# Kernel optimization log

Hardware: AMD Instinct MI355X
Metric: run time of the kernel (lower is better)

Reference implementation:

```python
import jax, jax.numpy as jnp
import numpy as np
from jax import lax

B_, L, D, EXPAND, N, R, K = 2, 1024, 1024, 2, 16, 64, 4
ED = EXPAND * D


def setup_inputs() -> dict:
    key = jax.random.key(0)
    ks = jax.random.split(key, 8)
    x = jax.random.normal(ks[0], (B_, L, D), dtype=jnp.float32)
    in_proj_w = jax.random.normal(ks[1], (2 * ED, D), dtype=jnp.float32) * (D ** -0.5)
    in_proj_b = jnp.zeros((2 * ED,), jnp.float32)
    conv_w = jax.random.normal(ks[2], (ED, 1, K), dtype=jnp.float32) * (K ** -0.5)
    conv_b = jnp.zeros((ED,), jnp.float32)
    x_proj_w = jax.random.normal(ks[3], (R + 2 * N, ED), dtype=jnp.float32) * (ED ** -0.5)
    dt_proj_w = jax.random.uniform(ks[4], (ED, R), jnp.float32, -(R ** -0.5), R ** -0.5)
    # inverse-softplus of dt ~ U[log(dt_min), log(dt_max)] (matches torch init)
    dt = jnp.exp(jax.random.uniform(ks[5], (ED,), jnp.float32) * (np.log(0.1) - np.log(0.001)) + np.log(0.001))
    dt_proj_b = dt + jnp.log(-jnp.expm1(-dt))  # softplus^{-1}(dt)
    A_log = jnp.log(jnp.broadcast_to(jnp.arange(1, N + 1, dtype=jnp.float32), (ED, N)))
    D_param = jnp.ones((ED,), jnp.float32)
    out_proj_w = jax.random.normal(ks[6], (D, ED), dtype=jnp.float32) * (ED ** -0.5)
    return {"x": x, "in_proj_w": in_proj_w, "in_proj_b": in_proj_b, "conv_w": conv_w,
            "conv_b": conv_b, "x_proj_w": x_proj_w, "dt_proj_w": dt_proj_w,
            "dt_proj_b": dt_proj_b, "A_log": A_log, "D_param": D_param,
            "out_proj_w": out_proj_w}


def _mamba_fwd(x, in_proj_w, in_proj_b, conv_w, conv_b, x_proj_w, dt_proj_w,
               dt_proj_b, A_log, D_param, out_proj_w):
    xz = x @ in_proj_w.T + in_proj_b                       # (B, L, 2*ED)
    xc, z = jnp.split(xz, 2, axis=-1)                      # (B, L, ED) each
    # causal depthwise conv over time (pad left K-1, valid)
    xc = xc.transpose(0, 2, 1)                             # (B, ED, L)
    xc = lax.conv_general_dilated(xc, conv_w, window_strides=(1,),
                                  padding=[(K - 1, 0)], feature_group_count=ED)
    xc = xc + conv_b[None, :, None]
    xc = jax.nn.silu(xc.transpose(0, 2, 1))                # (B, L, ED)
    # SSM params
    A = -jnp.exp(A_log)                                    # (ED, N)
    dbc = xc @ x_proj_w.T                                  # (B, L, R+2N)
    dt, Bmat, Cmat = jnp.split(dbc, [R, R + N], axis=-1)
    dt = jax.nn.softplus(dt @ dt_proj_w.T + dt_proj_b)     # (B, L, ED)
    dA = jnp.exp(dt[..., None] * A)                        # (B, L, ED, N)
    dBx = (dt * xc)[..., None] * Bmat[:, :, None, :]       # (B, L, ED, N)
    # parallel scan: h_t = dA_t * h_{t-1} + dBx_t
    def combine(e1, e2):
        a1, b1 = e1
        a2, b2 = e2
        return a1 * a2, a2 * b1 + b2
    _, hs = lax.associative_scan(combine, (dA, dBx), axis=1)  # (B, L, ED, N)
    y = jnp.einsum('bln,blen->ble', Cmat, hs) + D_param * xc  # (B, L, ED)
    out = (y * jax.nn.silu(z)) @ out_proj_w.T                 # (B, L, D)
    return out


def reference(x, in_proj_w, in_proj_b, conv_w, conv_b, x_proj_w, dt_proj_w,
              dt_proj_b, A_log, D_param, out_proj_w):
    return _mamba_fwd(x, in_proj_w, in_proj_b, conv_w, conv_b, x_proj_w,
                      dt_proj_w, dt_proj_b, A_log, D_param, out_proj_w)
```

## Files before the change

kernel.cpp:

```cpp
#include <hip/hip_runtime.h>
#include <cstddef>


#define BL   2048
#define DIM  1024
#define ED   2048
#define NST  16
#define RLOW 64
#define CH   64
#define LC   16
#define SK   16
#define DBCN 196608

typedef __attribute__((ext_vector_type(4))) float   f32x4;
typedef __attribute__((ext_vector_type(8))) __bf16  bf16x8;
typedef __attribute__((ext_vector_type(8))) unsigned short us8;

__device__ __forceinline__ float silu_(float x) {
  return x / (1.f + __expf(-x));
}

__device__ __forceinline__ unsigned short f2b(float x) {
  union { float f; unsigned int u; } v; v.f = x;
  unsigned int r = v.u + 0x7FFFu + ((v.u >> 16) & 1u);
  return (unsigned short)(r >> 16);
}

__device__ __forceinline__ float b2f(unsigned short u) {
  union { unsigned int i; float f; } v; v.i = (unsigned int)u << 16; return v.f;
}

__device__ __forceinline__ f32x4 mfma_bf16(us8 a, us8 b, f32x4 c) {
  return __builtin_amdgcn_mfma_f32_16x16x32_bf16(
      __builtin_bit_cast(bf16x8, a), __builtin_bit_cast(bf16x8, b), c, 0, 0, 0);
}

#define GLOAD_LDS16(gaddr, laddr)                                              \
  __builtin_amdgcn_global_load_lds(                                            \
      (const __attribute__((address_space(1))) unsigned int*)(gaddr),          \
      (__attribute__((address_space(3))) unsigned int*)(laddr), 16, 0, 0)

template <int BM, int BN, bool OBF>
__global__ __launch_bounds__(256) void gemm_bf16(
    const unsigned short* __restrict__ A,
    const unsigned short* __restrict__ W,
    const float* __restrict__ bias,
    void* __restrict__ Cp, int ldc, int Nout, int Kloop, int lda, int sstride)
{
  constexpr int BK  = 32;
  constexpr int FM  = BM / 32;
  constexpr int FN  = BN / 32;
  constexpr int NLA = BM / 64;
  constexpr int NLW = BN / 64;
  __shared__ unsigned short Alds[BM][BK];
  __shared__ unsigned short Wlds[BN][BK];

  const int tid  = threadIdx.x;
  const int w    = tid >> 6;
  const int lane = tid & 63;
  const int wr   = w >> 1, wc = w & 1;
  const int bm   = blockIdx.x * BM;
  const int bn   = blockIdx.y * BN;
  const int kb   = blockIdx.z * Kloop;

  f32x4 acc[FM][FN];
#pragma unroll
  for (int m = 0; m < FM; ++m)
#pragma unroll
    for (int n = 0; n < FN; ++n) acc[m][n] = (f32x4){0.f, 0.f, 0.f, 0.f};

  const int srow = w * 16 + (lane & 15);
  const int kq   = (lane >> 4) * 8;

  for (int k0 = 0; k0 < Kloop; k0 += BK) {
    __syncthreads();
#pragma unroll
    for (int j = 0; j < NLA; ++j)
      GLOAD_LDS16(A + (size_t)(bm + j * 64 + srow) * lda + kb + k0 + kq,
                  &Alds[j * 64 + w * 16][0]);
#pragma unroll
    for (int j = 0; j < NLW; ++j)
      GLOAD_LDS16(W + (size_t)(bn + j * 64 + srow) * lda + kb + k0 + kq,
                  &Wlds[j * 64 + w * 16][0]);
    __syncthreads();
    us8 af[FM], wf[FN];
#pragma unroll
    for (int m = 0; m < FM; ++m)
      af[m] = *(const us8*)(&Alds[0][0] + (wr * (BM / 2) + m * 16) * BK + lane * 8);
#pragma unroll
    for (int n = 0; n < FN; ++n)
      wf[n] = *(const us8*)(&Wlds[0][0] + (wc * (BN / 2) + n * 16) * BK + lane * 8);
#pragma unroll
    for (int m = 0; m < FM; ++m)
#pragma unroll
      for (int n = 0; n < FN; ++n)
        acc[m][n] = mfma_bf16(af[m], wf[n], acc[m][n]);
  }

  const int rbase = (lane >> 4) * 4;
  float* Cf = (float*)Cp + (size_t)blockIdx.z * sstride;
#pragma unroll
  for (int m = 0; m < FM; ++m) {
#pragma unroll
    for (int n = 0; n < FN; ++n) {
      const int col = bn + wc * (BN / 2) + n * 16 + (lane & 15);
      if (col < Nout) {
        const float bv = bias ? bias[col] : 0.f;
#pragma unroll
        for (int r = 0; r < 4; ++r) {
          const int row = bm + wr * (BM / 2) + m * 16 + rbase + r;
          const float v = acc[m][n][r] + bv;
          if (OBF) ((unsigned short*)Cp)[(size_t)row * ldc + col] = f2b(v);
          else     Cf[(size_t)row * ldc + col] = v;
        }
      }
    }
  }
}

__global__ __launch_bounds__(256) void reduce_dbc_k(
    const float* __restrict__ par, float* __restrict__ dbc)
{
  const int i = blockIdx.x * 256 + threadIdx.x;
  float4 s = ((const float4*)par)[i];
#pragma unroll
  for (int sk = 1; sk < SK; ++sk) {
    float4 v = ((const float4*)(par + (size_t)sk * DBCN))[i];
    s.x += v.x; s.y += v.y; s.z += v.z; s.w += v.w;
  }
  ((float4*)dbc)[i] = s;
}

template <int ACT>
__global__ __launch_bounds__(256) void gemm_nt(
    const float* __restrict__ A, int lda,
    const float* __restrict__ W, int ldw,
    const float* __restrict__ bias,
    float* __restrict__ C, int ldc,
    int N, int K)
{
  __shared__ float As[16][64];
  __shared__ float Ws[16][64];
  const int tid = threadIdx.x;
  const int bm = blockIdx.x * 64;
  const int bn = blockIdx.y * 64;
  const int tx = tid & 15;
  const int ty = tid >> 4;
  const int srow = tid >> 2;
  const int scg  = (tid & 3) * 4;

  float acc[4][4] = {};
  const float* Aptr = A + (size_t)(bm + srow) * lda + scg;
  const bool   wok  = (bn + srow) < N;
  const float* Wptr = W + (size_t)(bn + srow) * ldw + scg;

  for (int k0 = 0; k0 < K; k0 += 16) {
    float4 av = *(const float4*)(Aptr + k0);
    float4 wv = make_float4(0.f, 0.f, 0.f, 0.f);
    if (wok) wv = *(const float4*)(Wptr + k0);
    __syncthreads();
    As[scg + 0][srow] = av.x; As[scg + 1][srow] = av.y;
    As[scg + 2][srow] = av.z; As[scg + 3][srow] = av.w;
    Ws[scg + 0][srow] = wv.x; Ws[scg + 1][srow] = wv.y;
    Ws[scg + 2][srow] = wv.z; Ws[scg + 3][srow] = wv.w;
    __syncthreads();
#pragma unroll
    for (int k = 0; k < 16; ++k) {
      float4 a4 = *(const float4*)&As[k][ty * 4];
      float4 w4 = *(const float4*)&Ws[k][tx * 4];
      float a_[4] = {a4.x, a4.y, a4.z, a4.w};
      float w_[4] = {w4.x, w4.y, w4.z, w4.w};
#pragma unroll
      for (int i = 0; i < 4; ++i)
#pragma unroll
        for (int j = 0; j < 4; ++j)
          acc[i][j] += a_[i] * w_[j];
    }
  }

#pragma unroll
  for (int i = 0; i < 4; ++i) {
    const int row = bm + ty * 4 + i;
#pragma unroll
    for (int j = 0; j < 4; ++j) {
      const int col = bn + tx * 4 + j;
      if (col < N) {
        float v = acc[i][j];
        if (bias) v += bias[col];
        if (ACT == 1) v = (v > 20.f) ? v : log1pf(__expf(v));
        C[(size_t)row * ldc + col] = v;
      }
    }
  }
}

__global__ __launch_bounds__(256) void cvt_bf16_k(
    const float* __restrict__ in, unsigned short* __restrict__ out, int n4)
{
  const int i = blockIdx.x * 256 + threadIdx.x;
  if (i >= n4) return;
  float4 v = ((const float4*)in)[i];
  ushort4 o;
  o.x = f2b(v.x); o.y = f2b(v.y); o.z = f2b(v.z); o.w = f2b(v.w);
  ((ushort4*)out)[i] = o;
}

__global__ __launch_bounds__(256) void cvt_pad_xpw_k(
    const float* __restrict__ in, unsigned short* __restrict__ out)
{
  const int i = blockIdx.x * 256 + threadIdx.x;
  const int idx = i * 4;
  const int row = idx >> 11;
  ushort4 o = {0, 0, 0, 0};
  if (row < 96) {
    float4 v = *(const float4*)(in + idx);
    o.x = f2b(v.x); o.y = f2b(v.y); o.z = f2b(v.z); o.w = f2b(v.w);
  }
  *(ushort4*)(out + idx) = o;
}

__global__ __launch_bounds__(256) void conv_silu_k(
    const unsigned short* __restrict__ xzb, const float* __restrict__ cw,
    const float* __restrict__ cb, unsigned short* __restrict__ xcb)
{
  const int idx = blockIdx.x * 256 + threadIdx.x;
  const int row = idx >> 9;
  const int e   = (idx & 511) * 4;
  const int l   = row & 1023;
  const unsigned short* base = xzb + (size_t)(row - l) * (2 * ED) + e;

  float4 cbv = *(const float4*)(cb + e);
  float a0 = cbv.x, a1 = cbv.y, a2 = cbv.z, a3 = cbv.w;
#pragma unroll
  for (int k = 0; k < 4; ++k) {
    const int ls = l - 3 + k;
    if (ls >= 0) {
      ushort4 u = *(const ushort4*)(base + (size_t)ls * (2 * ED));
      a0 += cw[(size_t)(e + 0) * 4 + k] * b2f(u.x);
      a1 += cw[(size_t)(e + 1) * 4 + k] * b2f(u.y);
      a2 += cw[(size_t)(e + 2) * 4 + k] * b2f(u.z);
      a3 += cw[(size_t)(e + 3) * 4 + k] * b2f(u.w);
    }
  }
  ushort4 o;
  o.x = f2b(silu_(a0)); o.y = f2b(silu_(a1));
  o.z = f2b(silu_(a2)); o.w = f2b(silu_(a3));
  *(ushort4*)(xcb + (size_t)row * ED + e) = o;
}

__global__ __launch_bounds__(256, 4) void scan_phase1(
    const float* __restrict__ dt, const unsigned short* __restrict__ xcb,
    const float* __restrict__ dbc, const float* __restrict__ A_log,
    float* __restrict__ aprod_o, float* __restrict__ bfin_o)
{
  const int g  = blockIdx.x * 256 + threadIdx.x;
  const int e  = g & (ED - 1);
  const int bc = g >> 11;
  const int b  = bc >> 6;
  const int c  = bc & (CH - 1);
  const size_t rowbase = (size_t)b * 1024 + (size_t)c * LC;

  __shared__ float4 sB[LC][4];
  if (threadIdx.x < LC * 4) {
    const int row = threadIdx.x >> 2, q = threadIdx.x & 3;
    sB[row][q] = ((const float4*)(dbc + (rowbase + row) * 96 + RLOW))[q];
  }
  __syncthreads();

  float Aen[NST];
  {
    const float4* Ap = (const float4*)(A_log + (size_t)e * NST);
#pragma unroll
    for (int q = 0; q < 4; ++q) {
      float4 v = Ap[q];
      Aen[q*4+0] = -__expf(v.x); Aen[q*4+1] = -__expf(v.y);
      Aen[q*4+2] = -__expf(v.z); Aen[q*4+3] = -__expf(v.w);
    }
  }

  float dtv[LC], dxv[LC];
#pragma unroll
  for (int i = 0; i < LC; ++i) dtv[i] = dt[(rowbase + i) * ED + e];
#pragma unroll
  for (int i = 0; i < LC; ++i)
    dxv[i] = dtv[i] * b2f(xcb[(rowbase + i) * ED + e]);

  float h[NST], ap[NST];
#pragma unroll
  for (int n = 0; n < NST; ++n) { h[n] = 0.f; ap[n] = 1.f; }

  for (int i = 0; i < LC; ++i) {
    float Bv[NST];
#pragma unroll
    for (int q = 0; q < 4; ++q) {
      float4 v = sB[i][q];
      Bv[q*4+0]=v.x; Bv[q*4+1]=v.y; Bv[q*4+2]=v.z; Bv[q*4+3]=v.w;
    }
#pragma unroll
    for (int n = 0; n < NST; ++n) {
      const float dA = __expf(dtv[i] * Aen[n]);
      ap[n] *= dA;
      h[n] = fmaf(dA, h[n], dxv[i] * Bv[n]);
    }
  }

  const size_t obase = ((size_t)(b * ED + e) * CH + c) * NST;
  float4* ao = (float4*)(aprod_o + obase);
  float4* bo = (float4*)(bfin_o + obase);
#pragma unroll
  for (int q = 0; q < 4; ++q) {
    ao[q] = make_float4(ap[q*4+0], ap[q*4+1], ap[q*4+2], ap[q*4+3]);
    bo[q] = make_float4(h[q*4+0],  h[q*4+1],  h[q*4+2],  h[q*4+3]);
  }
}

__global__ __launch_bounds__(256) void scan_phase2(
    const float* __restrict__ aprod, float* __restrict__ bfin)
{
  const int be   = blockIdx.x * 4 + (threadIdx.x >> 6);
  const int lane = threadIdx.x & 63;
  const size_t base = (size_t)be * CH * NST;

  float Aa[NST], Bb[NST];
  {
    const float4* ap4 = (const float4*)(aprod + base);
    const float4* bp4 = (const float4*)(bfin + base);
#pragma unroll
    for (int q = 0; q < 4; ++q) {
      float4 v = ap4[lane * 4 + q];
      Aa[q*4+0]=v.x; Aa[q*4+1]=v.y; Aa[q*4+2]=v.z; Aa[q*4+3]=v.w;
      float4 w = bp4[lane * 4 + q];
      Bb[q*4+0]=w.x; Bb[q*4+1]=w.y; Bb[q*4+2]=w.z; Bb[q*4+3]=w.w;
    }
  }

#pragma unroll
  for (int d = 1; d < 64; d <<= 1) {
#pragma unroll
    for (int r = 0; r < NST; ++r) {
      const float aP = __shfl_up(Aa[r], d);
      const float bP = __shfl_up(Bb[r], d);
      if (lane >= d) {
        Bb[r] = fmaf(Aa[r], bP, Bb[r]);
        Aa[r] *= aP;
      }
    }
  }

#pragma unroll
  for (int r = 0; r < NST; ++r) {
    const float hs = __shfl_up(Bb[r], 1);
    Bb[r] = (lane == 0) ? 0.f : hs;
  }

  float4* ob4 = (float4*)(bfin + base);
#pragma unroll
  for (int q = 0; q < 4; ++q)
    ob4[lane * 4 + q] = make_float4(Bb[q*4+0], Bb[q*4+1], Bb[q*4+2], Bb[q*4+3]);
}

__global__ __launch_bounds__(256, 4) void scan_phase3(
    const float* __restrict__ dt, const unsigned short* __restrict__ xcb,
    const float* __restrict__ dbc, const float* __restrict__ A_log,
    const float* __restrict__ Dp, const unsigned short* __restrict__ xzb,
    const float* __restrict__ hst, unsigned short* __restrict__ ygb)
{
  const int g  = blockIdx.x * 256 + threadIdx.x;
  const int e  = g & (ED - 1);
  const int bc = g >> 11;
  const int b  = bc >> 6;
  const int c  = bc & (CH - 1);
  const size_t rowbase = (size_t)b * 1024 + (size_t)c * LC;

  __shared__ float4 sBC[LC][8];
  if (threadIdx.x < LC * 8) {
    const int row = threadIdx.x >> 3, q = threadIdx.x & 7;
    sBC[row][q] = ((const float4*)(dbc + (rowbase + row) * 96 + RLOW))[q];
  }
  __syncthreads();

  float Aen[NST];
  {
    const float4* Ap = (const float4*)(A_log + (size_t)e * NST);
#pragma unroll
    for (int q = 0; q < 4; ++q) {
      float4 v = Ap[q];
      Aen[q*4+0] = -__expf(v.x); Aen[q*4+1] = -__expf(v.y);
      Aen[q*4+2] = -__expf(v.z); Aen[q*4+3] = -__expf(v.w);
    }
  }

  float dtv[LC], xcv[LC];
#pragma unroll
  for (int i = 0; i < LC; ++i) dtv[i] = dt[(rowbase + i) * ED + e];
#pragma unroll
  for (int i = 0; i < LC; ++i) xcv[i] = b2f(xcb[(rowbase + i) * ED + e]);

  float h[NST];
  {
    const float4* Hp = (const float4*)(hst + ((size_t)(b * ED + e) * CH + c) * NST);
#pragma unroll
    for (int q = 0; q < 4; ++q) {
      float4 v = Hp[q];
      h[q*4+0]=v.x; h[q*4+1]=v.y; h[q*4+2]=v.z; h[q*4+3]=v.w;
    }
  }

  const float De = Dp[e];
  for (int i = 0; i < LC; ++i) {
    const size_t rr = rowbase + i;
    float Bv[NST], Cv[NST];
#pragma unroll
    for (int q = 0; q < 4; ++q) {
      float4 v = sBC[i][q];
      Bv[q*4+0]=v.x; Bv[q*4+1]=v.y; Bv[q*4+2]=v.z; Bv[q*4+3]=v.w;
      float4 w = sBC[i][q + 4];
      Cv[q*4+0]=w.x; Cv[q*4+1]=w.y; Cv[q*4+2]=w.z; Cv[q*4+3]=w.w;
    }
    const float dx = dtv[i] * xcv[i];
    float y = 0.f;
#pragma unroll
    for (int n = 0; n < NST; ++n) {
      const float dA = __expf(dtv[i] * Aen[n]);
      h[n] = fmaf(dA, h[n], dx * Bv[n]);
      y = fmaf(Cv[n], h[n], y);
    }
    y = fmaf(De, xcv[i], y);
    const float zf = b2f(xzb[rr * (2 * ED) + ED + e]);
    ygb[rr * ED + e] = f2b(y * silu_(zf));
  }
}

extern "C" void kernel_launch(void* const* d_in, const int* in_sizes, int n_in,
                              void* d_out, int out_size, void* d_ws, size_t ws_size,
                              hipStream_t stream) {
  const float* x         = (const float*)d_in[0];
  const float* in_w      = (const float*)d_in[1];
  const float* in_b      = (const float*)d_in[2];
  const float* conv_w    = (const float*)d_in[3];
  const float* conv_b    = (const float*)d_in[4];
  const float* xproj_w   = (const float*)d_in[5];
  const float* dtproj_w  = (const float*)d_in[6];
  const float* dtproj_b  = (const float*)d_in[7];
  const float* A_log     = (const float*)d_in[8];
  const float* D_param   = (const float*)d_in[9];
  const float* outproj_w = (const float*)d_in[10];
  float* out = (float*)d_out;

  float* ws    = (float*)d_ws;
  float* dbc   = ws;
  float* dtb   = dbc   + 196608;
  float* aprod = dtb   + 4194304;
  float* bfin  = aprod + 4194304;
  float* par   = bfin  + 4194304;
  unsigned short* xzb  = (unsigned short*)(par + 3145728);
  unsigned short* xb   = xzb  + 8388608;
  unsigned short* iwb  = xb   + 2097152;
  unsigned short* owb  = iwb  + 4194304;
  unsigned short* xpwb = owb  + 2097152;
  unsigned short* xcb  = xpwb + 262144;
  unsigned short* ygb  = xcb  + 4194304;

  const dim3 blk(256);

  cvt_bf16_k<<<dim3(2097152 / 4 / 256), blk, 0, stream>>>(x, xb, 2097152 / 4);
  cvt_bf16_k<<<dim3(4194304 / 4 / 256), blk, 0, stream>>>(in_w, iwb, 4194304 / 4);
  cvt_bf16_k<<<dim3(2097152 / 4 / 256), blk, 0, stream>>>(outproj_w, owb, 2097152 / 4);
  cvt_pad_xpw_k<<<dim3(262144 / 4 / 256), blk, 0, stream>>>(xproj_w, xpwb);

  gemm_bf16<128, 128, true><<<dim3(BL / 128, 4096 / 128), blk, 0, stream>>>(
      xb, iwb, in_b, xzb, 2 * ED, 2 * ED, DIM, DIM, 0);

  conv_silu_k<<<dim3((BL * (ED / 4)) / 256), blk, 0, stream>>>(
      xzb, conv_w, conv_b, xcb);

  gemm_bf16<128, 128, false><<<dim3(BL / 128, 1, SK), blk, 0, stream>>>(
      xcb, xpwb, nullptr, par, 96, 96, ED / SK, ED, DBCN);
  reduce_dbc_k<<<dim3(DBCN / 4 / 256), blk, 0, stream>>>(par, dbc);

  gemm_nt<1><<<dim3(BL / 64, ED / 64), blk, 0, stream>>>(
      dbc, 96, dtproj_w, RLOW, dtproj_b, dtb, ED, ED, RLOW);

  scan_phase1<<<dim3((2 * CH * ED) / 256), blk, 0, stream>>>(
      dtb, xcb, dbc, A_log, aprod, bfin);
  scan_phase2<<<dim3((2 * ED) / 4), blk, 0, stream>>>(aprod, bfin);
  scan_phase3<<<dim3((2 * CH * ED) / 256), blk, 0, stream>>>(
      dtb, xcb, dbc, A_log, D_param, xzb, bfin, ygb);

  gemm_bf16<64, 64, false><<<dim3(BL / 64, 1024 / 64), blk, 0, stream>>>(
      ygb, owb, nullptr, out, DIM, DIM, ED, ED, 0);
}
```

Measured before the change: 232.4 us.

## Double-buffer bf16 GEMM with BK=64, fuse conversions, split-K out_proj

The bf16 MFMA GEMM now uses BK=64 with double-buffered LDS, so the global-to-LDS load of the next tile is issued before the MFMAs on the current tile, and each iteration needs one barrier instead of two. The four fp32-to-bf16 conversion kernels are merged into one launch. The out_proj GEMM uses 64x128 tiles with a 2-way split-K into scratch (reusing the aprod buffer), followed by a small reduction kernel. This adds LDS use per block, which may lower occupancy, and adds an extra partial-sum write and reduction pass for the output.

```diff
diff --git a/kernel.cpp b/kernel.cpp
--- a/kernel.cpp
+++ b/kernel.cpp
@@ -47,13 +47,14 @@
     const float* __restrict__ bias,
     void* __restrict__ Cp, int ldc, int Nout, int Kloop, int lda, int sstride)
 {
-  constexpr int BK  = 32;
-  constexpr int FM  = BM / 32;
-  constexpr int FN  = BN / 32;
-  constexpr int NLA = BM / 64;
-  constexpr int NLW = BN / 64;
-  __shared__ unsigned short Alds[BM][BK];
-  __shared__ unsigned short Wlds[BN][BK];
+  constexpr int BK     = 64;
+  constexpr int FM     = BM / 32;
+  constexpr int FN     = BN / 32;
+  constexpr int NLA    = BM / 32;
+  constexpr int NLW    = BN / 32;
+  constexpr int ABYTES = BM * BK * 2;
+  constexpr int WBYTES = BN * BK * 2;
+  __shared__ char smem[2 * (ABYTES + WBYTES)];
 
   const int tid  = threadIdx.x;
   const int w    = tid >> 6;
@@ -69,33 +70,55 @@
 #pragma unroll
     for (int n = 0; n < FN; ++n) acc[m][n] = (f32x4){0.f, 0.f, 0.f, 0.f};
 
-  const int srow = w * 16 + (lane & 15);
-  const int kq   = (lane >> 4) * 8;
-
-  for (int k0 = 0; k0 < Kloop; k0 += BK) {
+  const int srow = ((tid >> 7) << 4) | (tid & 15);
+  const int kch  = (tid >> 4) & 7;
+  const int wofs = (tid >> 6) * 1024;
+
+  const unsigned short* Ag = A + (size_t)(bm + srow) * lda + kb + kch * 8;
+  const unsigned short* Wg = W + (size_t)(bn + srow) * lda + kb + kch * 8;
+
+#define STAGE(cur, k0)                                                         \
+  {                                                                            \
+    char* ab = smem + (cur) * (ABYTES + WBYTES);                               \
+    char* wb = ab + ABYTES;                                                    \
+    _Pragma("unroll")                                                          \
+    for (int j = 0; j < NLA; ++j)                                              \
+      GLOAD_LDS16(Ag + (size_t)(j * 32) * lda + (k0), ab + j * 4096 + wofs);   \
+    _Pragma("unroll")                                                          \
+    for (int j = 0; j < NLW; ++j)                                              \
+      GLOAD_LDS16(Wg + (size_t)(j * 32) * lda + (k0), wb + j * 4096 + wofs);   \
+  }
+
+  STAGE(0, 0);
+  int cur = 0;
+  const int NT = Kloop / BK;
+  for (int t = 0; t < NT; ++t) {
     __syncthreads();
-#pragma unroll
-    for (int j = 0; j < NLA; ++j)
-      GLOAD_LDS16(A + (size_t)(bm + j * 64 + srow) * lda + kb + k0 + kq,
-                  &Alds[j * 64 + w * 16][0]);
-#pragma unroll
-    for (int j = 0; j < NLW; ++j)
-      GLOAD_LDS16(W + (size_t)(bn + j * 64 + srow) * lda + kb + k0 + kq,
-                  &Wlds[j * 64 + w * 16][0]);
-    __syncthreads();
-    us8 af[FM], wf[FN];
+    if (t + 1 < NT) STAGE(cur ^ 1, (t + 1) * BK);
+
+    const char* ab = smem + cur * (ABYTES + WBYTES);
+    const char* wb = ab + ABYTES;
+    us8 af[FM][2], wf[FN][2];
 #pragma unroll
     for (int m = 0; m < FM; ++m)
-      af[m] = *(const us8*)(&Alds[0][0] + (wr * (BM / 2) + m * 16) * BK + lane * 8);
+#pragma unroll
+      for (int h = 0; h < 2; ++h)
+        af[m][h] = *(const us8*)(ab + (wr * FM + m) * 2048 + h * 1024 + lane * 16);
 #pragma unroll
     for (int n = 0; n < FN; ++n)
-      wf[n] = *(const us8*)(&Wlds[0][0] + (wc * (BN / 2) + n * 16) * BK + lane * 8);
-#pragma unroll
-    for (int m = 0; m < FM; ++m)
-#pragma unroll
-      for (int n = 0; n < FN; ++n)
-        acc[m][n] = mfma_bf16(af[m], wf[n], acc[m][n]);
-  }
+#pragma unroll
+      for (int h = 0; h < 2; ++h)
+        wf[n][h] = *(const us8*)(wb + (wc * FN + n) * 2048 + h * 1024 + lane * 16);
+#pragma unroll
+    for (int h = 0; h < 2; ++h)
+#pragma unroll
+      for (int m = 0; m < FM; ++m)
+#pragma unroll
+        for (int n = 0; n < FN; ++n)
+          acc[m][n] = mfma_bf16(af[m][h], wf[n][h], acc[m][n]);
+    cur ^= 1;
+  }
+#undef STAGE
 
   const int rbase = (lane >> 4) * 4;
   float* Cf = (float*)Cp + (size_t)blockIdx.z * sstride;
@@ -129,6 +152,16 @@
     s.x += v.x; s.y += v.y; s.z += v.z; s.w += v.w;
   }
   ((float4*)dbc)[i] = s;
+}
+
+__global__ __launch_bounds__(256) void reduce_out_k(
+    const float* __restrict__ par, float* __restrict__ out)
+{
+  const int i = blockIdx.x * 256 + threadIdx.x;
+  float4 a = ((const float4*)par)[i];
+  float4 b = ((const float4*)(par + 2097152))[i];
+  a.x += b.x; a.y += b.y; a.z += b.z; a.w += b.w;
+  ((float4*)out)[i] = a;
 }
 
 template <int ACT>
@@ -194,29 +227,32 @@
   }
 }
 
-__global__ __launch_bounds__(256) void cvt_bf16_k(
-    const float* __restrict__ in, unsigned short* __restrict__ out, int n4)
+__global__ __launch_bounds__(256) void cvt_all_k(
+    const float* __restrict__ x, const float* __restrict__ inw,
+    const float* __restrict__ ow, const float* __restrict__ xpw,
+    unsigned short* __restrict__ xb, unsigned short* __restrict__ iwb,
+    unsigned short* __restrict__ owb, unsigned short* __restrict__ xpwb)
 {
   const int i = blockIdx.x * 256 + threadIdx.x;
-  if (i >= n4) return;
-  float4 v = ((const float4*)in)[i];
+  const float* src; unsigned short* dst; int j;
+  if (i < 524288)       { src = x;   dst = xb;  j = i; }
+  else if (i < 1572864) { src = inw; dst = iwb; j = i - 524288; }
+  else if (i < 2097152) { src = ow;  dst = owb; j = i - 1572864; }
+  else {
+    j = i - 2097152;
+    const int idx = j * 4;
+    ushort4 o = {0, 0, 0, 0};
+    if ((idx >> 11) < 96) {
+      float4 v = *(const float4*)(xpw + idx);
+      o.x = f2b(v.x); o.y = f2b(v.y); o.z = f2b(v.z); o.w = f2b(v.w);
+    }
+    *(ushort4*)(xpwb + idx) = o;
+    return;
+  }
+  float4 v = ((const float4*)src)[j];
   ushort4 o;
   o.x = f2b(v.x); o.y = f2b(v.y); o.z = f2b(v.z); o.w = f2b(v.w);
-  ((ushort4*)out)[i] = o;
-}
-
-__global__ __launch_bounds__(256) void cvt_pad_xpw_k(
-    const float* __restrict__ in, unsigned short* __restrict__ out)
-{
-  const int i = blockIdx.x * 256 + threadIdx.x;
-  const int idx = i * 4;
-  const int row = idx >> 11;
-  ushort4 o = {0, 0, 0, 0};
-  if (row < 96) {
-    float4 v = *(const float4*)(in + idx);
-    o.x = f2b(v.x); o.y = f2b(v.y); o.z = f2b(v.z); o.w = f2b(v.w);
-  }
-  *(ushort4*)(out + idx) = o;
+  ((ushort4*)dst)[j] = o;
 }
 
 __global__ __launch_bounds__(256) void conv_silu_k(
@@ -452,21 +488,20 @@
   float* dtb   = dbc   + 196608;
   float* aprod = dtb   + 4194304;
   float* bfin  = aprod + 4194304;
-  float* par   = bfin  + 4194304;
-  unsigned short* xzb  = (unsigned short*)(par + 3145728);
+  float* parx  = bfin  + 4194304;
+  unsigned short* xzb  = (unsigned short*)(parx + 3145728);
   unsigned short* xb   = xzb  + 8388608;
   unsigned short* iwb  = xb   + 2097152;
   unsigned short* owb  = iwb  + 4194304;
   unsigned short* xpwb = owb  + 2097152;
   unsigned short* xcb  = xpwb + 262144;
   unsigned short* ygb  = xcb  + 4194304;
+  float* paro  = aprod;
 
   const dim3 blk(256);
 
-  cvt_bf16_k<<<dim3(2097152 / 4 / 256), blk, 0, stream>>>(x, xb, 2097152 / 4);
-  cvt_bf16_k<<<dim3(4194304 / 4 / 256), blk, 0, stream>>>(in_w, iwb, 4194304 / 4);
-  cvt_bf16_k<<<dim3(2097152 / 4 / 256), blk, 0, stream>>>(outproj_w, owb, 2097152 / 4);
-  cvt_pad_xpw_k<<<dim3(262144 / 4 / 256), blk, 0, stream>>>(xproj_w, xpwb);
+  cvt_all_k<<<dim3(2162688 / 256), blk, 0, stream>>>(
+      x, in_w, outproj_w, xproj_w, xb, iwb, owb, xpwb);
 
   gemm_bf16<128, 128, true><<<dim3(BL / 128, 4096 / 128), blk, 0, stream>>>(
       xb, iwb, in_b, xzb, 2 * ED, 2 * ED, DIM, DIM, 0);
@@ -475,8 +510,8 @@
       xzb, conv_w, conv_b, xcb);
 
   gemm_bf16<128, 128, false><<<dim3(BL / 128, 1, SK), blk, 0, stream>>>(
-      xcb, xpwb, nullptr, par, 96, 96, ED / SK, ED, DBCN);
-  reduce_dbc_k<<<dim3(DBCN / 4 / 256), blk, 0, stream>>>(par, dbc);
+      xcb, xpwb, nullptr, parx, 96, 96, ED / SK, ED, DBCN);
+  reduce_dbc_k<<<dim3(DBCN / 4 / 256), blk, 0, stream>>>(parx, dbc);
 
   gemm_nt<1><<<dim3(BL / 64, ED / 64), blk, 0, stream>>>(
       dbc, 96, dtproj_w, RLOW, dtproj_b, dtb, ED, ED, RLOW);
@@ -487,6 +522,7 @@
   scan_phase3<<<dim3((2 * CH * ED) / 256), blk, 0, stream>>>(
       dtb, xcb, dbc, A_log, D_param, xzb, bfin, ygb);
 
-  gemm_bf16<64, 64, false><<<dim3(BL / 64, 1024 / 64), blk, 0, stream>>>(
-      ygb, owb, nullptr, out, DIM, DIM, ED, ED, 0);
-}
+  gemm_bf16<64, 128, false><<<dim3(BL / 64, 1024 / 128, 2), blk, 0, stream>>>(
+      ygb, owb, nullptr, paro, DIM, DIM, ED / 2, ED, 2097152);
+  reduce_out_k<<<dim3(2097152 / 4 / 256), blk, 0, stream>>>(paro, out);
+}
```

Result: faster. 217.5 us (-6.4%).
